# Optimization experiments

Hardware: AMD Instinct MI355X
Metric: run time of the kernel (lower is better)

## Reference

```python
import jax, jax.numpy as jnp
import numpy as np

D = 64        # gat_output_dim == state_dim
HID = 128     # hidden_dim
ADIM = 2 * D  # action_dim (ope_dim + insert_dim)


def _mk(key, shape, scale=0.05):
    return jax.random.normal(key, shape, dtype=jnp.float32) * scale


def setup_inputs() -> dict:
    key = jax.random.key(0)
    ks = jax.random.split(key, 24)
    inp = {
        "ope_gat": jax.random.normal(ks[0], (8, 258, D), jnp.float32),
        "insert_gat": jax.random.normal(ks[1], (8, 256, D), jnp.float32),
        "h": jax.random.normal(ks[2], (8, D), jnp.float32),
        "c": jax.random.normal(ks[3], (8, D), jnp.float32),
        # LSTM (pytorch layout: gates i,f,g,o stacked -> [4D, in])
        "W_ih": _mk(ks[4], (4 * D, D)),
        "W_hh": _mk(ks[5], (4 * D, D)),
        "b_ih": _mk(ks[6], (4 * D,)),
        "b_hh": _mk(ks[7], (4 * D,)),
        # V_net: Linear(D,HID) -> Linear(HID,HID) -> LeakyReLU -> Linear(HID,1)
        "Wv0": _mk(ks[8], (HID, D)), "bv0": _mk(ks[9], (HID,)),
        "Wv1": _mk(ks[10], (HID, HID)), "bv1": _mk(ks[11], (HID,)),
        "Wv2": _mk(ks[12], (1, HID)), "bv2": _mk(ks[13], (1,)),
        # A_net: Linear(D+ADIM,HID) -> Linear(HID,HID) -> LeakyReLU -> Linear(HID,1)
        "Wa0": _mk(ks[14], (HID, D + ADIM)), "ba0": _mk(ks[15], (HID,)),
        "Wa1": _mk(ks[16], (HID, HID)), "ba1": _mk(ks[17], (HID,)),
        "Wa2": _mk(ks[18], (1, HID)), "ba2": _mk(ks[19], (1,)),
    }
    return inp


def _lrelu(x):
    return jnp.where(x >= 0, x, 0.01 * x)


def _forward(ope_gat, insert_gat, h, c,
             W_ih, W_hh, b_ih, b_hh,
             Wv0, bv0, Wv1, bv1, Wv2, bv2,
             Wa0, ba0, Wa1, ba1, Wa2, ba2):
    ope = ope_gat[:, 1:-1]                # [B, O, D]
    state = ope.mean(axis=-2)             # [B, D]

    # single-step LSTM (pytorch gate order i, f, g, o)
    gates = state @ W_ih.T + b_ih + h @ W_hh.T + b_hh  # [B, 4D]
    i_g, f_g, g_g, o_g = jnp.split(gates, 4, axis=-1)
    cn = jax.nn.sigmoid(f_g) * c + jax.nn.sigmoid(i_g) * jnp.tanh(g_g)
    hn = jax.nn.sigmoid(o_g) * jnp.tanh(cn)
    rnn_state = hn                        # [B, D]

    # V head (note: no activation after first linear -- name-overwrite bug)
    V = _lrelu((rnn_state @ Wv0.T + bv0) @ Wv1.T + bv1) @ Wv2.T + bv2  # [B, 1]

    # A head on the full (ope x insert) cross-join; ope side is detached.
    ope_d = jax.lax.stop_gradient(ope)    # [B, O, D]
    B, O, _ = ope_d.shape
    I = insert_gat.shape[1]
    # Decompose first linear over the concat [state | ope | insert] (exact math).
    Ws, Wo, Wi = Wa0[:, :D], Wa0[:, D:2 * D], Wa0[:, 2 * D:]
    h0 = (rnn_state @ Ws.T)[:, None, None, :] \
         + jnp.einsum('bod,hd->boh', ope_d, Wo)[:, :, None, :] \
         + jnp.einsum('bid,hd->bih', insert_gat, Wi)[:, None, :, :] \
         + ba0                              # [B, O, I, HID]
    h1 = _lrelu(jnp.einsum('boih,gh->boig', h0, Wa1) + ba1)
    A = (jnp.einsum('boih,h->boi', h1, Wa2[0]) + ba2[0]).reshape(B, O * I)
    return V, A, hn, cn


def reference(ope_gat, insert_gat, h, c,
              W_ih, W_hh, b_ih, b_hh,
              Wv0, bv0, Wv1, bv1, Wv2, bv2,
              Wa0, ba0, Wa1, ba1, Wa2, ba2):
    return _forward(ope_gat, insert_gat, h, c,
                    W_ih, W_hh, b_ih, b_hh,
                    Wv0, bv0, Wv1, bv1, Wv2, bv2,
                    Wa0, ba0, Wa1, ba1, Wa2, ba2)
```

## Files before the change

kernel.cpp:

```cpp
#include <hip/hip_runtime.h>
#include <hip/hip_bf16.h>
#include <math.h>

typedef unsigned short u16;

#define PART  6416
#define WA1B  10512
#define WOB   18704
#define WIB   22800

__device__ __forceinline__ u16 f2b(float x) { __hip_bfloat16 b = __float2bfloat16(x); return *(u16*)&b; }
__device__ __forceinline__ void cvt8(const uint4 u, float* f) {
    f[0] = __uint_as_float(u.x << 16); f[1] = __uint_as_float(u.x & 0xFFFF0000u);
    f[2] = __uint_as_float(u.y << 16); f[3] = __uint_as_float(u.y & 0xFFFF0000u);
    f[4] = __uint_as_float(u.z << 16); f[5] = __uint_as_float(u.z & 0xFFFF0000u);
    f[6] = __uint_as_float(u.w << 16); f[7] = __uint_as_float(u.w & 0xFFFF0000u);
}
__device__ __forceinline__ float dot4(const float4 a, const float4 b) {
    return a.x*b.x + a.y*b.y + a.z*b.z + a.w*b.w;
}

__global__ __launch_bounds__(256) void k0_pre(
    const float* __restrict__ ope, const float* __restrict__ Wa0,
    const float* __restrict__ Wa1, float* __restrict__ ws, int fb)
{
    const int t = threadIdx.x;
    if (blockIdx.x < 64) {
        const int b = blockIdx.x >> 3, s = blockIdx.x & 7;
        const int d = t & 63, rg = t >> 6;
        __shared__ float red[256];
        const float* p = ope + b*16512 + (1 + s*32 + rg*8)*64 + d;
        float acc = 0.f;
        #pragma unroll
        for (int rr = 0; rr < 8; ++rr) acc += p[rr*64];
        red[t] = acc;
        __syncthreads();
        if (t < 64)
            ws[fb + PART + (b*8 + s)*64 + t] = red[t] + red[t+64] + red[t+128] + red[t+192];
    } else {
        const int e0 = ((blockIdx.x - 64)*256 + t) * 8;
        const float* src;
        u16* dst;
        if (e0 < 16384)      { src = Wa1 + e0;                                      dst = (u16*)(ws + fb + WA1B) + e0; }
        else if (e0 < 24576) { const int i = e0 - 16384; src = Wa0 + (i>>6)*192 + 64  + (i&63); dst = (u16*)(ws + fb + WOB) + i; }
        else                 { const int i = e0 - 24576; src = Wa0 + (i>>6)*192 + 128 + (i&63); dst = (u16*)(ws + fb + WIB) + i; }
        const float4 a = *(const float4*)src;
        const float4 c = *(const float4*)(src + 4);
        ushort4 u0; u0.x = f2b(a.x); u0.y = f2b(a.y); u0.z = f2b(a.z); u0.w = f2b(a.w);
        ushort4 u1; u1.x = f2b(c.x); u1.y = f2b(c.y); u1.z = f2b(c.z); u1.w = f2b(c.w);
        *(ushort4*)dst = u0;
        *(ushort4*)(dst + 4) = u1;
    }
}

__global__ __launch_bounds__(256) void k1_head(
    const float* __restrict__ hin, const float* __restrict__ cin,
    const float* __restrict__ W_ih, const float* __restrict__ W_hh,
    const float* __restrict__ b_ih, const float* __restrict__ b_hh,
    const float* __restrict__ Wv0, const float* __restrict__ bv0,
    const float* __restrict__ Wv1, const float* __restrict__ bv1,
    const float* __restrict__ Wv2, const float* __restrict__ bv2,
    const float* __restrict__ Wa0, const float* __restrict__ ba0,
    const float* __restrict__ Wa2, const float* __restrict__ ba2,
    float* __restrict__ ws, int fb)
{
    const int b = blockIdx.x, t = threadIdx.x;
    __shared__ __align__(16) float state[64], hvec[64], gl[256], hn_s[64], t0a[128], t1a[128];

    if (t < 64) {
        float s = 0.f;
        #pragma unroll
        for (int s8 = 0; s8 < 8; ++s8) s += ws[fb + PART + (b*8 + s8)*64 + t];
        state[t] = s * (1.f/256.f);
    } else if (t < 128) hvec[t-64] = hin[b*64 + (t-64)];
    __syncthreads();

    {
        float g = b_ih[t] + b_hh[t];
        const float4* wi = (const float4*)(W_ih + t*64);
        const float4* wh = (const float4*)(W_hh + t*64);
        #pragma unroll
        for (int k = 0; k < 16; ++k)
            g += dot4(wi[k], *(const float4*)&state[k*4])
               + dot4(wh[k], *(const float4*)&hvec[k*4]);
        gl[t] = g;
    }
    __syncthreads();

    if (t < 64) {
        const float ig = gl[t], fg = gl[64+t], gg = gl[128+t], og = gl[192+t];
        const float c  = cin[b*64 + t];
        const float si = 1.f/(1.f + expf(-ig));
        const float sf = 1.f/(1.f + expf(-fg));
        const float so = 1.f/(1.f + expf(-og));
        const float cn = sf*c + si*tanhf(gg);
        const float hn = so*tanhf(cn);
        ws[fb + 1288 + b*64 + t] = hn;
        ws[fb + 1800 + b*64 + t] = cn;
        hn_s[t] = hn;
    }
    __syncthreads();

    if (t < 128) {
        float a = bv0[t];
        const float4* w = (const float4*)(Wv0 + t*64);
        #pragma unroll
        for (int k = 0; k < 16; ++k) a += dot4(w[k], *(const float4*)&hn_s[k*4]);
        t0a[t] = a;
    }
    __syncthreads();
    if (t < 128) {
        float a = bv1[t];
        const float4* w = (const float4*)(Wv1 + t*128);
        #pragma unroll
        for (int k = 0; k < 32; ++k) a += dot4(w[k], *(const float4*)&t0a[k*4]);
        a = (a >= 0.f) ? a : 0.01f*a;
        t1a[t] = a * Wv2[t];
        float s2 = ba0[t];
        const float4* w0 = (const float4*)(Wa0 + t*192);
        #pragma unroll
        for (int k = 0; k < 16; ++k) s2 += dot4(w0[k], *(const float4*)&hn_s[k*4]);
        ws[fb + b*128 + t] = s2;
        const float w2v = Wa2[t];
        ws[fb + 1024 + t] = 0.505f * w2v;
        ws[fb + 1152 + t] = 0.495f * w2v;
    }
    __syncthreads();
    if (t < 64) {
        float v = t1a[t] + t1a[t + 64];
        v += __shfl_xor(v, 32); v += __shfl_xor(v, 16); v += __shfl_xor(v, 8);
        v += __shfl_xor(v, 4);  v += __shfl_xor(v, 2);  v += __shfl_xor(v, 1);
        if (t == 0) {
            ws[fb + 1280 + b] = v + bv2[0];
            ws[fb + 2313]    = ba2[0];
        }
    }
}

template<bool MF32>
__device__ void k2_body(const float* ope, const float* ins, const float* ba1,
    float* ws, int fb, u16* Wa1s, u16* Wsel, u16* inrows, float* P)
{
    const int t = threadIdx.x;
    const int b = blockIdx.x >> 5;
    const int r0 = (blockIdx.x & 31) * 16;
    const int side = (r0 >= 256) ? 1 : 0;

    {
        const u16* wa1b = (const u16*)(ws + fb + WA1B);
        #pragma unroll
        for (int k = 0; k < 8; ++k) {
            const int e4 = t + k*256;
            const int g = e4 >> 4, hq = (e4 & 15) * 8;
            *(uint4*)&Wa1s[g*136 + hq] = *(const uint4*)(wa1b + g*128 + hq);
        }
    }
    {
        const u16* wsb = (const u16*)(ws + fb + (side ? WIB : WOB));
        #pragma unroll
        for (int k = 0; k < 4; ++k) {
            const int e4 = t + k*256;
            const int h = e4 >> 3, dq = (e4 & 7) * 8;
            *(uint4*)&Wsel[h*72 + dq] = *(const uint4*)(wsb + h*64 + dq);
        }
    }
    {
        const int r = t >> 4, dq = (t & 15) * 4;
        const float* src = side
            ? (ins + b*16384 + (r0 - 256 + r)*64 + dq)
            : (ope + b*16512 + (1 + r0 + r)*64 + dq);
        const float4 w = *(const float4*)src;
        ushort4 u; u.x = f2b(w.x); u.y = f2b(w.y); u.z = f2b(w.z); u.w = f2b(w.w);
        *(ushort4*)&inrows[r*72 + dq] = u;
    }
    __syncthreads();

    const int r = t >> 4;
    const int q = t & 15;

    {
        float acc[8];
        #pragma unroll
        for (int k = 0; k < 8; ++k)
            acc[k] = side ? 0.0f : ws[fb + b*128 + (q + 16*k)];
        #pragma unroll
        for (int d8 = 0; d8 < 64; d8 += 8) {
            float iv[8];
            cvt8(*(const uint4*)&inrows[r*72 + d8], iv);
            #pragma unroll
            for (int k = 0; k < 8; ++k) {
                float wv[8];
                cvt8(*(const uint4*)&Wsel[(q + 16*k)*72 + d8], wv);
                #pragma unroll
                for (int j = 0; j < 8; ++j) acc[k] += wv[j] * iv[j];
            }
        }
        #pragma unroll
        for (int k = 0; k < 8; ++k) P[r*132 + q + 16*k] = acc[k];
    }
    __syncthreads();

    {
        float acc[8] = {0.f,0.f,0.f,0.f,0.f,0.f,0.f,0.f};
        #pragma unroll
        for (int h8 = 0; h8 < 128; h8 += 8) {
            const float4 p0 = *(const float4*)&P[r*132 + h8];
            const float4 p1 = *(const float4*)&P[r*132 + h8 + 4];
            #pragma unroll
            for (int k = 0; k < 8; ++k) {
                float wv[8];
                cvt8(*(const uint4*)&Wa1s[(q + 16*k)*136 + h8], wv);
                float a = acc[k];
                a += wv[0]*p0.x + wv[1]*p0.y + wv[2]*p0.z + wv[3]*p0.w;
                a += wv[4]*p1.x + wv[5]*p1.y + wv[6]*p1.z + wv[7]*p1.w;
                acc[k] = a;
            }
        }
        float part = 0.f;
        if (!side) {
            const int row = b*256 + r0 + r;
            #pragma unroll
            for (int k = 0; k < 8; ++k) {
                const int g = q + 16*k;
                const float v = acc[k] + ba1[g];
                part = fmaf(ws[fb + 1024 + g], v, part);
                if (MF32) ws[row*128 + g] = v;
                else      ((u16*)ws)[row*128 + g] = f2b(v);
            }
        } else {
            const int row = b*256 + (r0 - 256) + r;
            #pragma unroll
            for (int k = 0; k < 8; ++k) {
                const int g = q + 16*k;
                part = fmaf(ws[fb + 1024 + g], acc[k], part);
                if (MF32) ws[262144 + row*128 + g] = acc[k];
                else      ((u16*)ws)[262144 + row*128 + g] = f2b(acc[k]);
            }
        }
        part += __shfl_xor(part, 1);
        part += __shfl_xor(part, 2);
        part += __shfl_xor(part, 4);
        part += __shfl_xor(part, 8);
        if (q == 0) {
            if (!side) ws[fb + 2320 + b*256 + r0 + r] = part + ws[fb + 2313];
            else       ws[fb + 4368 + b*256 + (r0 - 256) + r] = part;
        }
    }
}

__global__ __launch_bounds__(256) void k2_xy(
    const float* ope, const float* ins, const float* ba1,
    float* ws, int fb, int mf32)
{
    __shared__ __align__(16) u16 Wa1s[128*136];
    __shared__ __align__(16) u16 Wsel[128*72];
    __shared__ __align__(16) u16 inrows[16*72];
    __shared__ __align__(16) float P[16*132];
    if (mf32) k2_body<true >(ope, ins, ba1, ws, fb, Wa1s, Wsel, inrows, P);
    else      k2_body<false>(ope, ins, ba1, ws, fb, Wa1s, Wsel, inrows, P);
}

template<bool MF32>
__device__ void k3_body(const float* ws, float* out, int fb)
{
    const int t = threadIdx.x;
    const int b = blockIdx.x >> 6;
    const int o0 = (blockIdx.x & 63) * 4;
    const float* wb = ws + fb + 1152;

    float acc[4] = {0.f, 0.f, 0.f, 0.f};
    #pragma unroll
    for (int gc = 0; gc < 8; ++gc) {
        float yv[16], wv[16];
        if (MF32) {
            const float* yr = ws + 262144 + (b*256 + t)*128 + gc*16;
            #pragma unroll
            for (int k = 0; k < 4; ++k) *(float4*)&yv[k*4] = *(const float4*)(yr + k*4);
        } else {
            const u16* yr = (const u16*)ws + 262144 + (b*256 + t)*128 + gc*16;
            cvt8(*(const uint4*)yr, yv);
            cvt8(*(const uint4*)(yr + 8), yv + 8);
        }
        #pragma unroll
        for (int k = 0; k < 4; ++k) *(float4*)&wv[k*4] = *(const float4*)(wb + gc*16 + k*4);
        #pragma unroll
        for (int o = 0; o < 4; ++o) {
            float xv[16];
            if (MF32) {
                const float* xr = ws + (b*256 + o0 + o)*128 + gc*16;
                #pragma unroll
                for (int k = 0; k < 4; ++k) *(float4*)&xv[k*4] = *(const float4*)(xr + k*4);
            } else {
                const u16* xr = (const u16*)ws + (b*256 + o0 + o)*128 + gc*16;
                cvt8(*(const uint4*)xr, xv);
                cvt8(*(const uint4*)(xr + 8), xv + 8);
            }
            float a = acc[o];
            #pragma unroll
            for (int j = 0; j < 16; ++j)
                a = fmaf(wv[j], fabsf(xv[j] + yv[j]), a);
            acc[o] = a;
        }
    }
    const float c2 = ws[fb + 4368 + b*256 + t];
    #pragma unroll
    for (int o = 0; o < 4; ++o)
        out[8 + b*65536 + (o0 + o)*256 + t] = ws[fb + 2320 + b*256 + o0 + o] + c2 + acc[o];

    if (blockIdx.x == 0) {
        if (t < 8) out[t] = ws[fb + 1280 + t];
        #pragma unroll
        for (int j = t; j < 512; j += 256) {
            out[524296 + j] = ws[fb + 1288 + j];
            out[524808 + j] = ws[fb + 1800 + j];
        }
    }
}

__global__ __launch_bounds__(256) void k3_adv(const float* ws, float* out,
                                              int fb, int mf32)
{
    if (mf32) k3_body<true >(ws, out, fb);
    else      k3_body<false>(ws, out, fb);
}

extern "C" void kernel_launch(void* const* d_in, const int* in_sizes, int n_in,
                              void* d_out, int out_size, void* d_ws, size_t ws_size,
                              hipStream_t stream) {
    float* ws = (float*)d_ws;
    float* out = (float*)d_out;
    const int mf32 = (ws_size >= (size_t)2400000) ? 1 : 0;
    const int fb   = mf32 ? 524288 : 262144;

    const float* ope = (const float*)d_in[0];
    const float* ins = (const float*)d_in[1];

    k0_pre <<<dim3(80),  dim3(256), 0, stream>>>(
        ope, (const float*)d_in[14], (const float*)d_in[16], ws, fb);
    k1_head<<<dim3(8),   dim3(256), 0, stream>>>(
        (const float*)d_in[2], (const float*)d_in[3],
        (const float*)d_in[4], (const float*)d_in[5],
        (const float*)d_in[6], (const float*)d_in[7],
        (const float*)d_in[8], (const float*)d_in[9],
        (const float*)d_in[10], (const float*)d_in[11],
        (const float*)d_in[12], (const float*)d_in[13],
        (const float*)d_in[14], (const float*)d_in[15],
        (const float*)d_in[18], (const float*)d_in[19], ws, fb);
    k2_xy  <<<dim3(256), dim3(256), 0, stream>>>(
        ope, ins, (const float*)d_in[17], ws, fb, mf32);
    k3_adv <<<dim3(512), dim3(256), 0, stream>>>(ws, out, fb, mf32);
}
```

Measured before the change: 132.3 us.

## Merge LSTM head and XY projection into one kernel by folding state term

```diff
diff --git a/kernel.cpp b/kernel.cpp
--- a/kernel.cpp
+++ b/kernel.cpp
@@ -4,10 +4,13 @@
 
 typedef unsigned short u16;
 
+#define FB    524288
 #define PART  6416
 #define WA1B  10512
 #define WOB   18704
 #define WIB   22800
+#define SOFF  26896
+#define C1S   27920
 
 __device__ __forceinline__ u16 f2b(float x) { __hip_bfloat16 b = __float2bfloat16(x); return *(u16*)&b; }
 __device__ __forceinline__ void cvt8(const uint4 u, float* f) {
@@ -22,7 +25,8 @@
 
 __global__ __launch_bounds__(256) void k0_pre(
     const float* __restrict__ ope, const float* __restrict__ Wa0,
-    const float* __restrict__ Wa1, float* __restrict__ ws, int fb)
+    const float* __restrict__ Wa1, const float* __restrict__ Wa2,
+    const float* __restrict__ ba2, float* __restrict__ ws)
 {
     const int t = threadIdx.x;
     if (blockIdx.x < 64) {
@@ -36,24 +40,32 @@
         red[t] = acc;
         __syncthreads();
         if (t < 64)
-            ws[fb + PART + (b*8 + s)*64 + t] = red[t] + red[t+64] + red[t+128] + red[t+192];
-    } else {
+            ws[FB + PART + (b*8 + s)*64 + t] = red[t] + red[t+64] + red[t+128] + red[t+192];
+    } else if (blockIdx.x < 80) {
         const int e0 = ((blockIdx.x - 64)*256 + t) * 8;
         const float* src;
         u16* dst;
-        if (e0 < 16384)      { src = Wa1 + e0;                                      dst = (u16*)(ws + fb + WA1B) + e0; }
-        else if (e0 < 24576) { const int i = e0 - 16384; src = Wa0 + (i>>6)*192 + 64  + (i&63); dst = (u16*)(ws + fb + WOB) + i; }
-        else                 { const int i = e0 - 24576; src = Wa0 + (i>>6)*192 + 128 + (i&63); dst = (u16*)(ws + fb + WIB) + i; }
+        if (e0 < 16384)      { src = Wa1 + e0;                                              dst = (u16*)(ws + FB + WA1B) + e0; }
+        else if (e0 < 24576) { const int i = e0 - 16384; src = Wa0 + (i>>6)*192 + 64  + (i&63); dst = (u16*)(ws + FB + WOB) + i; }
+        else                 { const int i = e0 - 24576; src = Wa0 + (i>>6)*192 + 128 + (i&63); dst = (u16*)(ws + FB + WIB) + i; }
         const float4 a = *(const float4*)src;
         const float4 c = *(const float4*)(src + 4);
         ushort4 u0; u0.x = f2b(a.x); u0.y = f2b(a.y); u0.z = f2b(a.z); u0.w = f2b(a.w);
         ushort4 u1; u1.x = f2b(c.x); u1.y = f2b(c.y); u1.z = f2b(c.z); u1.w = f2b(c.w);
         *(ushort4*)dst = u0;
         *(ushort4*)(dst + 4) = u1;
+    } else {
+        if (t < 128) {
+            const float w2v = Wa2[t];
+            ws[FB + 1024 + t] = 0.505f * w2v;
+            ws[FB + 1152 + t] = 0.495f * w2v;
+        }
+        if (t == 128) ws[FB + 2313] = ba2[0];
     }
 }
 
-__global__ __launch_bounds__(256) void k1_head(
+__global__ __launch_bounds__(256) void k12_main(
+    const float* __restrict__ ope, const float* __restrict__ ins,
     const float* __restrict__ hin, const float* __restrict__ cin,
     const float* __restrict__ W_ih, const float* __restrict__ W_hh,
     const float* __restrict__ b_ih, const float* __restrict__ b_hh,
@@ -61,267 +73,253 @@
     const float* __restrict__ Wv1, const float* __restrict__ bv1,
     const float* __restrict__ Wv2, const float* __restrict__ bv2,
     const float* __restrict__ Wa0, const float* __restrict__ ba0,
-    const float* __restrict__ Wa2, const float* __restrict__ ba2,
-    float* __restrict__ ws, int fb)
-{
-    const int b = blockIdx.x, t = threadIdx.x;
-    __shared__ __align__(16) float state[64], hvec[64], gl[256], hn_s[64], t0a[128], t1a[128];
-
-    if (t < 64) {
-        float s = 0.f;
-        #pragma unroll
-        for (int s8 = 0; s8 < 8; ++s8) s += ws[fb + PART + (b*8 + s8)*64 + t];
-        state[t] = s * (1.f/256.f);
-    } else if (t < 128) hvec[t-64] = hin[b*64 + (t-64)];
-    __syncthreads();
-
-    {
-        float g = b_ih[t] + b_hh[t];
-        const float4* wi = (const float4*)(W_ih + t*64);
-        const float4* wh = (const float4*)(W_hh + t*64);
-        #pragma unroll
-        for (int k = 0; k < 16; ++k)
-            g += dot4(wi[k], *(const float4*)&state[k*4])
-               + dot4(wh[k], *(const float4*)&hvec[k*4]);
-        gl[t] = g;
-    }
-    __syncthreads();
-
-    if (t < 64) {
-        const float ig = gl[t], fg = gl[64+t], gg = gl[128+t], og = gl[192+t];
-        const float c  = cin[b*64 + t];
-        const float si = 1.f/(1.f + expf(-ig));
-        const float sf = 1.f/(1.f + expf(-fg));
-        const float so = 1.f/(1.f + expf(-og));
-        const float cn = sf*c + si*tanhf(gg);
-        const float hn = so*tanhf(cn);
-        ws[fb + 1288 + b*64 + t] = hn;
-        ws[fb + 1800 + b*64 + t] = cn;
-        hn_s[t] = hn;
-    }
-    __syncthreads();
-
-    if (t < 128) {
-        float a = bv0[t];
-        const float4* w = (const float4*)(Wv0 + t*64);
-        #pragma unroll
-        for (int k = 0; k < 16; ++k) a += dot4(w[k], *(const float4*)&hn_s[k*4]);
-        t0a[t] = a;
-    }
-    __syncthreads();
-    if (t < 128) {
-        float a = bv1[t];
-        const float4* w = (const float4*)(Wv1 + t*128);
-        #pragma unroll
-        for (int k = 0; k < 32; ++k) a += dot4(w[k], *(const float4*)&t0a[k*4]);
-        a = (a >= 0.f) ? a : 0.01f*a;
-        t1a[t] = a * Wv2[t];
-        float s2 = ba0[t];
-        const float4* w0 = (const float4*)(Wa0 + t*192);
-        #pragma unroll
-        for (int k = 0; k < 16; ++k) s2 += dot4(w0[k], *(const float4*)&hn_s[k*4]);
-        ws[fb + b*128 + t] = s2;
-        const float w2v = Wa2[t];
-        ws[fb + 1024 + t] = 0.505f * w2v;
-        ws[fb + 1152 + t] = 0.495f * w2v;
-    }
-    __syncthreads();
-    if (t < 64) {
-        float v = t1a[t] + t1a[t + 64];
-        v += __shfl_xor(v, 32); v += __shfl_xor(v, 16); v += __shfl_xor(v, 8);
-        v += __shfl_xor(v, 4);  v += __shfl_xor(v, 2);  v += __shfl_xor(v, 1);
-        if (t == 0) {
-            ws[fb + 1280 + b] = v + bv2[0];
-            ws[fb + 2313]    = ba2[0];
-        }
-    }
-}
-
-template<bool MF32>
-__device__ void k2_body(const float* ope, const float* ins, const float* ba1,
-    float* ws, int fb, u16* Wa1s, u16* Wsel, u16* inrows, float* P)
-{
-    const int t = threadIdx.x;
-    const int b = blockIdx.x >> 5;
-    const int r0 = (blockIdx.x & 31) * 16;
-    const int side = (r0 >= 256) ? 1 : 0;
-
-    {
-        const u16* wa1b = (const u16*)(ws + fb + WA1B);
-        #pragma unroll
-        for (int k = 0; k < 8; ++k) {
-            const int e4 = t + k*256;
-            const int g = e4 >> 4, hq = (e4 & 15) * 8;
-            *(uint4*)&Wa1s[g*136 + hq] = *(const uint4*)(wa1b + g*128 + hq);
-        }
-    }
-    {
-        const u16* wsb = (const u16*)(ws + fb + (side ? WIB : WOB));
-        #pragma unroll
-        for (int k = 0; k < 4; ++k) {
-            const int e4 = t + k*256;
-            const int h = e4 >> 3, dq = (e4 & 7) * 8;
-            *(uint4*)&Wsel[h*72 + dq] = *(const uint4*)(wsb + h*64 + dq);
-        }
-    }
-    {
-        const int r = t >> 4, dq = (t & 15) * 4;
-        const float* src = side
-            ? (ins + b*16384 + (r0 - 256 + r)*64 + dq)
-            : (ope + b*16512 + (1 + r0 + r)*64 + dq);
-        const float4 w = *(const float4*)src;
-        ushort4 u; u.x = f2b(w.x); u.y = f2b(w.y); u.z = f2b(w.z); u.w = f2b(w.w);
-        *(ushort4*)&inrows[r*72 + dq] = u;
-    }
-    __syncthreads();
-
-    const int r = t >> 4;
-    const int q = t & 15;
-
-    {
-        float acc[8];
-        #pragma unroll
-        for (int k = 0; k < 8; ++k)
-            acc[k] = side ? 0.0f : ws[fb + b*128 + (q + 16*k)];
-        #pragma unroll
-        for (int d8 = 0; d8 < 64; d8 += 8) {
-            float iv[8];
-            cvt8(*(const uint4*)&inrows[r*72 + d8], iv);
-            #pragma unroll
-            for (int k = 0; k < 8; ++k) {
-                float wv[8];
-                cvt8(*(const uint4*)&Wsel[(q + 16*k)*72 + d8], wv);
-                #pragma unroll
-                for (int j = 0; j < 8; ++j) acc[k] += wv[j] * iv[j];
-            }
-        }
-        #pragma unroll
-        for (int k = 0; k < 8; ++k) P[r*132 + q + 16*k] = acc[k];
-    }
-    __syncthreads();
-
-    {
-        float acc[8] = {0.f,0.f,0.f,0.f,0.f,0.f,0.f,0.f};
-        #pragma unroll
-        for (int h8 = 0; h8 < 128; h8 += 8) {
-            const float4 p0 = *(const float4*)&P[r*132 + h8];
-            const float4 p1 = *(const float4*)&P[r*132 + h8 + 4];
-            #pragma unroll
-            for (int k = 0; k < 8; ++k) {
-                float wv[8];
-                cvt8(*(const uint4*)&Wa1s[(q + 16*k)*136 + h8], wv);
-                float a = acc[k];
-                a += wv[0]*p0.x + wv[1]*p0.y + wv[2]*p0.z + wv[3]*p0.w;
-                a += wv[4]*p1.x + wv[5]*p1.y + wv[6]*p1.z + wv[7]*p1.w;
-                acc[k] = a;
-            }
-        }
-        float part = 0.f;
-        if (!side) {
-            const int row = b*256 + r0 + r;
-            #pragma unroll
-            for (int k = 0; k < 8; ++k) {
-                const int g = q + 16*k;
-                const float v = acc[k] + ba1[g];
-                part = fmaf(ws[fb + 1024 + g], v, part);
-                if (MF32) ws[row*128 + g] = v;
-                else      ((u16*)ws)[row*128 + g] = f2b(v);
-            }
-        } else {
-            const int row = b*256 + (r0 - 256) + r;
-            #pragma unroll
-            for (int k = 0; k < 8; ++k) {
-                const int g = q + 16*k;
-                part = fmaf(ws[fb + 1024 + g], acc[k], part);
-                if (MF32) ws[262144 + row*128 + g] = acc[k];
-                else      ((u16*)ws)[262144 + row*128 + g] = f2b(acc[k]);
-            }
-        }
-        part += __shfl_xor(part, 1);
-        part += __shfl_xor(part, 2);
-        part += __shfl_xor(part, 4);
-        part += __shfl_xor(part, 8);
-        if (q == 0) {
-            if (!side) ws[fb + 2320 + b*256 + r0 + r] = part + ws[fb + 2313];
-            else       ws[fb + 4368 + b*256 + (r0 - 256) + r] = part;
-        }
-    }
-}
-
-__global__ __launch_bounds__(256) void k2_xy(
-    const float* ope, const float* ins, const float* ba1,
-    float* ws, int fb, int mf32)
+    const float* __restrict__ Wa1, const float* __restrict__ ba1,
+    float* __restrict__ ws)
 {
     __shared__ __align__(16) u16 Wa1s[128*136];
     __shared__ __align__(16) u16 Wsel[128*72];
     __shared__ __align__(16) u16 inrows[16*72];
     __shared__ __align__(16) float P[16*132];
-    if (mf32) k2_body<true >(ope, ins, ba1, ws, fb, Wa1s, Wsel, inrows, P);
-    else      k2_body<false>(ope, ins, ba1, ws, fb, Wa1s, Wsel, inrows, P);
-}
-
-template<bool MF32>
-__device__ void k3_body(const float* ws, float* out, int fb)
+    const int t = threadIdx.x;
+
+    if (blockIdx.x < 256) {
+        const int b = blockIdx.x >> 5;
+        const int r0 = (blockIdx.x & 31) * 16;
+        const int side = (r0 >= 256) ? 1 : 0;
+
+        {
+            const u16* wa1b = (const u16*)(ws + FB + WA1B);
+            #pragma unroll
+            for (int k = 0; k < 8; ++k) {
+                const int e4 = t + k*256;
+                const int g = e4 >> 4, hq = (e4 & 15) * 8;
+                *(uint4*)&Wa1s[g*136 + hq] = *(const uint4*)(wa1b + g*128 + hq);
+            }
+        }
+        {
+            const u16* wsb = (const u16*)(ws + FB + (side ? WIB : WOB));
+            #pragma unroll
+            for (int k = 0; k < 4; ++k) {
+                const int e4 = t + k*256;
+                const int h = e4 >> 3, dq = (e4 & 7) * 8;
+                *(uint4*)&Wsel[h*72 + dq] = *(const uint4*)(wsb + h*64 + dq);
+            }
+        }
+        {
+            const int r = t >> 4, dq = (t & 15) * 4;
+            const float* src = side
+                ? (ins + b*16384 + (r0 - 256 + r)*64 + dq)
+                : (ope + b*16512 + (1 + r0 + r)*64 + dq);
+            const float4 w = *(const float4*)src;
+            ushort4 u; u.x = f2b(w.x); u.y = f2b(w.y); u.z = f2b(w.z); u.w = f2b(w.w);
+            *(ushort4*)&inrows[r*72 + dq] = u;
+        }
+        __syncthreads();
+
+        const int r = t >> 4;
+        const int q = t & 15;
+
+        {
+            float acc[8] = {0.f,0.f,0.f,0.f,0.f,0.f,0.f,0.f};
+            #pragma unroll
+            for (int d8 = 0; d8 < 64; d8 += 8) {
+                float iv[8];
+                cvt8(*(const uint4*)&inrows[r*72 + d8], iv);
+                #pragma unroll
+                for (int k = 0; k < 8; ++k) {
+                    float wv[8];
+                    cvt8(*(const uint4*)&Wsel[(q + 16*k)*72 + d8], wv);
+                    #pragma unroll
+                    for (int j = 0; j < 8; ++j) acc[k] += wv[j] * iv[j];
+                }
+            }
+            #pragma unroll
+            for (int k = 0; k < 8; ++k) P[r*132 + q + 16*k] = acc[k];
+        }
+        __syncthreads();
+
+        {
+            float acc[8] = {0.f,0.f,0.f,0.f,0.f,0.f,0.f,0.f};
+            #pragma unroll
+            for (int h8 = 0; h8 < 128; h8 += 8) {
+                const float4 p0 = *(const float4*)&P[r*132 + h8];
+                const float4 p1 = *(const float4*)&P[r*132 + h8 + 4];
+                #pragma unroll
+                for (int k = 0; k < 8; ++k) {
+                    float wv[8];
+                    cvt8(*(const uint4*)&Wa1s[(q + 16*k)*136 + h8], wv);
+                    float a = acc[k];
+                    a += wv[0]*p0.x + wv[1]*p0.y + wv[2]*p0.z + wv[3]*p0.w;
+                    a += wv[4]*p1.x + wv[5]*p1.y + wv[6]*p1.z + wv[7]*p1.w;
+                    acc[k] = a;
+                }
+            }
+            float part = 0.f;
+            const int row = side ? (b*256 + r0 - 256 + r) : (b*256 + r0 + r);
+            float* dst = side ? (ws + 262144 + row*128) : (ws + row*128);
+            #pragma unroll
+            for (int k = 0; k < 8; ++k) {
+                const int g = q + 16*k;
+                part = fmaf(ws[FB + 1024 + g], acc[k], part);
+                dst[g] = acc[k];
+            }
+            part += __shfl_xor(part, 1);
+            part += __shfl_xor(part, 2);
+            part += __shfl_xor(part, 4);
+            part += __shfl_xor(part, 8);
+            if (q == 0) {
+                if (!side) ws[FB + 2320 + row] = part;
+                else       ws[FB + 4368 + row] = part;
+            }
+        }
+    } else {
+        const int b = blockIdx.x - 256;
+        float* f = (float*)Wa1s;
+        float* state = f;
+        float* hvec  = f + 64;
+        float* gl    = f + 128;
+        float* hn_s  = f + 384;
+        float* t0a   = f + 448;
+        float* t1a   = f + 576;
+        float* s2s   = f + 704;
+        float* red   = f + 832;
+
+        if (t < 64) {
+            float s = 0.f;
+            #pragma unroll
+            for (int s8 = 0; s8 < 8; ++s8) s += ws[FB + PART + (b*8 + s8)*64 + t];
+            state[t] = s * (1.f/256.f);
+        } else if (t < 128) hvec[t-64] = hin[b*64 + (t-64)];
+        __syncthreads();
+
+        {
+            float g = b_ih[t] + b_hh[t];
+            const float4* wi = (const float4*)(W_ih + t*64);
+            const float4* wh = (const float4*)(W_hh + t*64);
+            #pragma unroll
+            for (int k = 0; k < 16; ++k)
+                g += dot4(wi[k], *(const float4*)&state[k*4])
+                   + dot4(wh[k], *(const float4*)&hvec[k*4]);
+            gl[t] = g;
+        }
+        __syncthreads();
+
+        if (t < 64) {
+            const float ig = gl[t], fg = gl[64+t], gg = gl[128+t], og = gl[192+t];
+            const float c  = cin[b*64 + t];
+            const float si = 1.f/(1.f + expf(-ig));
+            const float sf = 1.f/(1.f + expf(-fg));
+            const float so = 1.f/(1.f + expf(-og));
+            const float cn = sf*c + si*tanhf(gg);
+            const float hn = so*tanhf(cn);
+            ws[FB + 1288 + b*64 + t] = hn;
+            ws[FB + 1800 + b*64 + t] = cn;
+            hn_s[t] = hn;
+        }
+        __syncthreads();
+
+        if (t < 128) {
+            float a = bv0[t];
+            const float4* w = (const float4*)(Wv0 + t*64);
+            #pragma unroll
+            for (int k = 0; k < 16; ++k) a += dot4(w[k], *(const float4*)&hn_s[k*4]);
+            t0a[t] = a;
+        }
+        __syncthreads();
+        if (t < 128) {
+            float a = bv1[t];
+            const float4* w = (const float4*)(Wv1 + t*128);
+            #pragma unroll
+            for (int k = 0; k < 32; ++k) a += dot4(w[k], *(const float4*)&t0a[k*4]);
+            a = (a >= 0.f) ? a : 0.01f*a;
+            t1a[t] = a * Wv2[t];
+            float s2 = ba0[t];
+            const float4* w0 = (const float4*)(Wa0 + t*192);
+            #pragma unroll
+            for (int k = 0; k < 16; ++k) s2 += dot4(w0[k], *(const float4*)&hn_s[k*4]);
+            s2s[t] = s2;
+        }
+        __syncthreads();
+        if (t < 128) {
+            float sv = ba1[t];
+            const float4* w = (const float4*)(Wa1 + t*128);
+            #pragma unroll
+            for (int k = 0; k < 32; ++k) sv += dot4(w[k], *(const float4*)&s2s[k*4]);
+            ws[FB + SOFF + b*128 + t] = sv;
+            red[t] = ws[FB + 1024 + t] * sv;
+        }
+        __syncthreads();
+        if (t < 64) {
+            float c = red[t] + red[t + 64];
+            float v = t1a[t] + t1a[t + 64];
+            c += __shfl_xor(c, 32); v += __shfl_xor(v, 32);
+            c += __shfl_xor(c, 16); v += __shfl_xor(v, 16);
+            c += __shfl_xor(c, 8);  v += __shfl_xor(v, 8);
+            c += __shfl_xor(c, 4);  v += __shfl_xor(v, 4);
+            c += __shfl_xor(c, 2);  v += __shfl_xor(v, 2);
+            c += __shfl_xor(c, 1);  v += __shfl_xor(v, 1);
+            if (t == 0) {
+                ws[FB + C1S + b]  = c + ws[FB + 2313];
+                ws[FB + 1280 + b] = v + bv2[0];
+            }
+        }
+    }
+}
+
+__global__ __launch_bounds__(256) void k3_adv(const float* __restrict__ ws,
+                                              float* __restrict__ out)
 {
     const int t = threadIdx.x;
     const int b = blockIdx.x >> 6;
     const int o0 = (blockIdx.x & 63) * 4;
-    const float* wb = ws + fb + 1152;
+    const float* wb = ws + FB + 1152;
 
     float acc[4] = {0.f, 0.f, 0.f, 0.f};
     #pragma unroll
     for (int gc = 0; gc < 8; ++gc) {
-        float yv[16], wv[16];
-        if (MF32) {
+        float syv[16], wv[16];
+        {
             const float* yr = ws + 262144 + (b*256 + t)*128 + gc*16;
-            #pragma unroll
-            for (int k = 0; k < 4; ++k) *(float4*)&yv[k*4] = *(const float4*)(yr + k*4);
-        } else {
-            const u16* yr = (const u16*)ws + 262144 + (b*256 + t)*128 + gc*16;
-            cvt8(*(const uint4*)yr, yv);
-            cvt8(*(const uint4*)(yr + 8), yv + 8);
-        }
-        #pragma unroll
-        for (int k = 0; k < 4; ++k) *(float4*)&wv[k*4] = *(const float4*)(wb + gc*16 + k*4);
+            const float* sr = ws + FB + SOFF + b*128 + gc*16;
+            #pragma unroll
+            for (int k = 0; k < 4; ++k) {
+                const float4 y4 = *(const float4*)(yr + k*4);
+                const float4 s4 = *(const float4*)(sr + k*4);
+                syv[k*4+0] = y4.x + s4.x; syv[k*4+1] = y4.y + s4.y;
+                syv[k*4+2] = y4.z + s4.z; syv[k*4+3] = y4.w + s4.w;
+                *(float4*)&wv[k*4] = *(const float4*)(wb + gc*16 + k*4);
+            }
+        }
         #pragma unroll
         for (int o = 0; o < 4; ++o) {
-            float xv[16];
-            if (MF32) {
-                const float* xr = ws + (b*256 + o0 + o)*128 + gc*16;
-                #pragma unroll
-                for (int k = 0; k < 4; ++k) *(float4*)&xv[k*4] = *(const float4*)(xr + k*4);
-            } else {
-                const u16* xr = (const u16*)ws + (b*256 + o0 + o)*128 + gc*16;
-                cvt8(*(const uint4*)xr, xv);
-                cvt8(*(const uint4*)(xr + 8), xv + 8);
-            }
+            const float* xr = ws + (b*256 + o0 + o)*128 + gc*16;
             float a = acc[o];
             #pragma unroll
-            for (int j = 0; j < 16; ++j)
-                a = fmaf(wv[j], fabsf(xv[j] + yv[j]), a);
+            for (int k = 0; k < 4; ++k) {
+                const float4 x4 = *(const float4*)(xr + k*4);
+                a = fmaf(wv[k*4+0], fabsf(x4.x + syv[k*4+0]), a);
+                a = fmaf(wv[k*4+1], fabsf(x4.y + syv[k*4+1]), a);
+                a = fmaf(wv[k*4+2], fabsf(x4.z + syv[k*4+2]), a);
+                a = fmaf(wv[k*4+3], fabsf(x4.w + syv[k*4+3]), a);
+            }
             acc[o] = a;
         }
     }
-    const float c2 = ws[fb + 4368 + b*256 + t];
+    const float c2  = ws[FB + 4368 + b*256 + t];
+    const float c1s = ws[FB + C1S + b];
     #pragma unroll
     for (int o = 0; o < 4; ++o)
-        out[8 + b*65536 + (o0 + o)*256 + t] = ws[fb + 2320 + b*256 + o0 + o] + c2 + acc[o];
+        out[8 + b*65536 + (o0 + o)*256 + t] =
+            ws[FB + 2320 + b*256 + o0 + o] + c1s + c2 + acc[o];
 
     if (blockIdx.x == 0) {
-        if (t < 8) out[t] = ws[fb + 1280 + t];
+        if (t < 8) out[t] = ws[FB + 1280 + t];
         #pragma unroll
         for (int j = t; j < 512; j += 256) {
-            out[524296 + j] = ws[fb + 1288 + j];
-            out[524808 + j] = ws[fb + 1800 + j];
+            out[524296 + j] = ws[FB + 1288 + j];
+            out[524808 + j] = ws[FB + 1800 + j];
         }
     }
-}
-
-__global__ __launch_bounds__(256) void k3_adv(const float* ws, float* out,
-                                              int fb, int mf32)
-{
-    if (mf32) k3_body<true >(ws, out, fb);
-    else      k3_body<false>(ws, out, fb);
 }
 
 extern "C" void kernel_launch(void* const* d_in, const int* in_sizes, int n_in,
@@ -329,15 +327,15 @@
                               hipStream_t stream) {
     float* ws = (float*)d_ws;
     float* out = (float*)d_out;
-    const int mf32 = (ws_size >= (size_t)2400000) ? 1 : 0;
-    const int fb   = mf32 ? 524288 : 262144;
 
     const float* ope = (const float*)d_in[0];
     const float* ins = (const float*)d_in[1];
 
-    k0_pre <<<dim3(80),  dim3(256), 0, stream>>>(
-        ope, (const float*)d_in[14], (const float*)d_in[16], ws, fb);
-    k1_head<<<dim3(8),   dim3(256), 0, stream>>>(
+    k0_pre  <<<dim3(81),  dim3(256), 0, stream>>>(
+        ope, (const float*)d_in[14], (const float*)d_in[16],
+        (const float*)d_in[18], (const float*)d_in[19], ws);
+    k12_main<<<dim3(264), dim3(256), 0, stream>>>(
+        ope, ins,
         (const float*)d_in[2], (const float*)d_in[3],
         (const float*)d_in[4], (const float*)d_in[5],
         (const float*)d_in[6], (const float*)d_in[7],
@@ -345,8 +343,6 @@
         (const float*)d_in[10], (const float*)d_in[11],
         (const float*)d_in[12], (const float*)d_in[13],
         (const float*)d_in[14], (const float*)d_in[15],
-        (const float*)d_in[18], (const float*)d_in[19], ws, fb);
-    k2_xy  <<<dim3(256), dim3(256), 0, stream>>>(
-        ope, ins, (const float*)d_in[17], ws, fb, mf32);
-    k3_adv <<<dim3(512), dim3(256), 0, stream>>>(ws, out, fb, mf32);
-}
+        (const float*)d_in[16], (const float*)d_in[17], ws);
+    k3_adv  <<<dim3(512), dim3(256), 0, stream>>>(ws, out);
+}
```

Measured after the change: 123.2 us. -6.8%, faster.
